# Kernel tuning notes

Hardware: AMD Instinct MI355X
Metric: run time of the kernel (lower is better)

Reference implementation:

```python
import jax, jax.numpy as jnp
import numpy as np

B, T, S, F_IN, F_OUT, K, L = 8, 8, 500, 32, 64, 3, 3


def setup_inputs() -> dict:
    key = jax.random.key(0)
    ks = jax.random.split(key, 10)
    x = jax.random.normal(ks[0], (B, T, S, F_IN), dtype=jnp.float32)
    Adj_t = jax.random.uniform(ks[1], (T, T), dtype=jnp.float32)
    Adj_s = jax.random.uniform(ks[2], (S, S), dtype=jnp.float32)
    # small mixing coefficients so Adj^k stays numerically tame
    s = jax.random.uniform(ks[3], (4,), dtype=jnp.float32) * 0.005
    H = jax.random.normal(ks[4], (L, K, F_OUT, F_OUT), dtype=jnp.float32) / jnp.sqrt(F_OUT)
    W1 = jax.random.normal(ks[5], (F_OUT, F_IN), dtype=jnp.float32) / jnp.sqrt(F_IN)
    b1 = jax.random.normal(ks[6], (F_OUT,), dtype=jnp.float32) * 0.01
    W2 = jax.random.normal(ks[7], (F_OUT, F_OUT), dtype=jnp.float32) / jnp.sqrt(F_OUT)
    b2 = jax.random.normal(ks[8], (F_OUT,), dtype=jnp.float32) * 0.01
    merge = jax.random.normal(ks[9], (T,), dtype=jnp.float32)
    return {"x": x, "Adj_t": Adj_t, "Adj_s": Adj_s, "s": s, "H": H,
            "W1": W1, "b1": b1, "W2": W2, "b2": b2, "merge": merge}


def reference(x, Adj_t, Adj_s, s, H, W1, b1, W2, b2, merge):
    Bx, Tx, Sx, Fin = x.shape
    N = Tx * Sx
    n_layers, Kk = H.shape[0], H.shape[1]
    I_t = jnp.eye(Tx, dtype=x.dtype)
    I_s = jnp.eye(Sx, dtype=x.dtype)
    I_st = jnp.eye(N, dtype=x.dtype)
    # mixed Kronecker product-graph adjacency, (T*S) x (T*S)
    Adj = (s[0] * I_st
           + s[1] * jnp.kron(I_t, Adj_s)
           + s[2] * jnp.kron(Adj_t, I_s)
           + s[3] * jnp.kron(Adj_t, Adj_s))
    # cache Adj^k for k = 0..K-1 (same math as per-layer matrix_power)
    powers = [I_st]
    for _ in range(1, Kk):
        powers.append(powers[-1] @ Adj)
    xf = x.reshape(Bx, N, Fin) @ W1.T + b1  # [B, N, F_out]
    for l in range(n_layers):
        acc = jnp.zeros_like(xf)
        for k in range(Kk):
            acc = acc + jnp.einsum('nm,bmf->bnf', powers[k], xf) @ H[l, k]
        xf = jnp.tanh(acc)
    xf = xf @ W2.T + b2  # [B, N, F_out]
    xo = xf.reshape(Bx, Tx, Sx, -1)  # [B, T, S, F_out]
    # transpose(3,1) -> [B,F,S,T]; matmul(merge) contracts T; transpose(2,1) -> [B,S,F]
    return jnp.einsum('btsf,t->bsf', xo, merge)
```

## Files before the change

kernel.cpp:

```cpp
#include <hip/hip_runtime.h>

#define BB 8
#define TT 8
#define SS 500
#define SP 512
#define FIN 32
#define FF 64
#define NBT 64
#define KT 1536
#define LROW_S 136
#define HROW 200
#define AROW 1544
#define WROW 196
#define OROW 520

typedef short bf16x8 __attribute__((ext_vector_type(8)));
typedef float floatx4 __attribute__((ext_vector_type(4)));

__device__ __forceinline__ unsigned f2bf(float x) {
    unsigned u = __builtin_bit_cast(unsigned, x);
    return (u + 0x7FFFu + ((u >> 16) & 1u)) >> 16;
}
__device__ __forceinline__ float bf2f(unsigned short h) {
    unsigned u = ((unsigned)h) << 16;
    return __builtin_bit_cast(float, u);
}
__device__ __forceinline__ float ftanh(float x) {
    float ax = fabsf(x);
    float e = __expf(-2.f * ax);
    float r = (1.f - e) * __builtin_amdgcn_rcpf(1.f + e);
    return copysignf(r, x);
}

__device__ __forceinline__ void ctab(int m, float s0, float s1, float s2, float s3,
                                     float& c0, float& c1, float& c2) {
    c0 = 0.f; c1 = 0.f; c2 = 0.f;
    switch (m) {
        case 0: c0 = 1.f; c1 = s0; c2 = s0 * s0; break;
        case 1: c1 = s1; c2 = 2.f * s0 * s1; break;
        case 2: c2 = s1 * s1; break;
        case 3: c1 = s2; c2 = 2.f * s0 * s2; break;
        case 4: c1 = s3; c2 = 2.f * (s0 * s3 + s1 * s2); break;
        case 5: c2 = 2.f * s1 * s3; break;
        case 6: c2 = s2 * s2; break;
        case 7: c2 = 2.f * s2 * s3; break;
        case 8: c2 = s3 * s3; break;
    }
}

__global__ __launch_bounds__(256) void setup_k(const float* __restrict__ x,
                                               const float* __restrict__ W1,
                                               const float* __restrict__ b1,
                                               const float* __restrict__ As,
                                               const float* __restrict__ At,
                                               const float* __restrict__ sc,
                                               const float* __restrict__ H,
                                               unsigned short* __restrict__ Asb,
                                               unsigned short* __restrict__ AsbT,
                                               unsigned short* __restrict__ HcT,
                                               float* __restrict__ CtT,
                                               unsigned short* __restrict__ xfT,
                                               unsigned short* __restrict__ Abig0) {
    int tid = threadIdx.x;
    if (blockIdx.x < 512) {
        __shared__ float Xs[64][FIN + 1];
        __shared__ float Wl[FIN][FF];
        __shared__ float Ot[64][FF + 1];
        __shared__ float bl[FF];
        int bt = blockIdx.x >> 3, s0 = (blockIdx.x & 7) * 64;
        int b = bt >> 3, t = bt & 7;

        for (int i = tid; i < FIN * FF; i += 256) { int f = i >> 5, j = i & 31; Wl[j][f] = W1[i]; }
        if (tid < FF) bl[tid] = b1[tid];
        const float* xb = x + (size_t)bt * SS * FIN;
        #pragma unroll
        for (int i = 0; i < 8; ++i) {
            int lin = i * 256 + tid; int r = lin >> 5, j = lin & 31;
            int s = s0 + r;
            Xs[r][j] = (s < SS) ? xb[(size_t)s * FIN + j] : 0.f;
        }
        __syncthreads();
        int f = tid & 63, sq = tid >> 6;
        for (int i = 0; i < 16; ++i) {
            int r = sq * 16 + i;
            float acc = bl[f];
            #pragma unroll
            for (int j = 0; j < FIN; ++j) acc += Xs[r][j] * Wl[j][f];
            Ot[r][f] = (s0 + r < SS) ? acc : 0.f;
        }
        __syncthreads();
        #pragma unroll
        for (int it = 0; it < 2; ++it) {
            int idx = it * 256 + tid;
            int row = idx >> 3, c = idx & 7;
            int4 w;
            unsigned short tmp[8];
            #pragma unroll
            for (int q = 0; q < 8; ++q) tmp[q] = (unsigned short)f2bf(Ot[row][c * 8 + q]);
            w.x = tmp[0] | (tmp[1] << 16); w.y = tmp[2] | (tmp[3] << 16);
            w.z = tmp[4] | (tmp[5] << 16); w.w = tmp[6] | (tmp[7] << 16);
            *(int4*)(Abig0 + (size_t)(b * SP + s0 + row) * KT + t * 192 + c * 8) = w;
        }
        {
            int ff = tid >> 2, scol = (tid & 3) * 16;
            unsigned short tmp[16];
            #pragma unroll
            for (int i = 0; i < 16; ++i) tmp[i] = (unsigned short)f2bf(Ot[scol + i][ff]);
            unsigned short* dp = xfT + ((size_t)bt * FF + ff) * SP + s0 + scol;
            #pragma unroll
            for (int q = 0; q < 2; ++q) {
                int4 w;
                w.x = tmp[q*8+0] | (tmp[q*8+1] << 16); w.y = tmp[q*8+2] | (tmp[q*8+3] << 16);
                w.z = tmp[q*8+4] | (tmp[q*8+5] << 16); w.w = tmp[q*8+6] | (tmp[q*8+7] << 16);
                *(int4*)(dp + q * 8) = w;
            }
        }
        return;
    }
    int idx = (blockIdx.x - 512) * 256 + tid;
    if (idx < 262144) {
        int s = idx >> 9, k = idx & 511;
        Asb[idx] = (s < SS && k < SS) ? (unsigned short)f2bf(As[(size_t)s * SS + k]) : 0;
    } else if (idx < 524288) {
        int r = idx - 262144;
        int j = r >> 9, k = r & 511;
        AsbT[r] = (j < SS && k < SS) ? (unsigned short)f2bf(As[(size_t)k * SS + j]) : 0;
    } else {
        int r = idx - 524288;
        if (r < 110592) {
            int l = r / 36864;
            int r2 = r - l * 36864;
            int row = r2 / 192;
            int col = r2 - row * 192;
            int p = row >> 6, f = row & 63;
            int bp = col >> 6, j = col & 63;
            float s0 = sc[0], s1 = sc[1], s2 = sc[2], s3 = sc[3];
            float c0, c1, c2;
            ctab(p * 3 + bp, s0, s1, s2, s3, c0, c1, c2);
            float val = c0 * H[((size_t)(l * 3 + 0) * 64 + j) * 64 + f]
                      + c1 * H[((size_t)(l * 3 + 1) * 64 + j) * 64 + f]
                      + c2 * H[((size_t)(l * 3 + 2) * 64 + j) * 64 + f];
            HcT[r] = (unsigned short)f2bf(val);
        } else if (r < 110784) {
            int i2 = r - 110592;
            int pt = i2 >> 3, t = i2 & 7;
            int p = pt >> 3, tp = pt & 7;
            float val;
            if (p == 0) val = (t == tp) ? 1.f : 0.f;
            else if (p == 1) val = At[t * 8 + tp];
            else {
                val = 0.f;
                #pragma unroll
                for (int kk = 0; kk < 8; ++kk) val += At[t * 8 + kk] * At[kk * 8 + tp];
            }
            CtT[i2] = val;
        }
    }
}

__global__ __launch_bounds__(256) void prep2_k(const unsigned short* __restrict__ Asb,
                                               const unsigned short* __restrict__ AsbT,
                                               unsigned short* __restrict__ Asqb) {
    int tid = threadIdx.x;
    int wave = tid >> 6, lane = tid & 63;
    int l16 = lane & 15, quad = lane >> 4;
    int st = blockIdx.x, ct = blockIdx.y;

    const unsigned short* ap = Asb + (size_t)(st * 16 + l16) * SP + quad * 8;
    const unsigned short* bp = AsbT + (size_t)(ct * 64 + wave * 16 + l16) * SP + quad * 8;
    floatx4 acc = {};
    #pragma unroll 4
    for (int k0 = 0; k0 < SP; k0 += 32)
        acc = __builtin_amdgcn_mfma_f32_16x16x32_bf16(*(const bf16x8*)(ap + k0),
                                                      *(const bf16x8*)(bp + k0), acc, 0, 0, 0);
    int j = ct * 64 + wave * 16 + l16;
    int i0 = st * 16 + quad * 4;
    #pragma unroll
    for (int r = 0; r < 4; ++r)
        Asqb[(size_t)(i0 + r) * SP + j] = (unsigned short)f2bf(acc[r]);
}

__global__ __launch_bounds__(256) void smm_k(const unsigned short* __restrict__ Asb,
                                             const unsigned short* __restrict__ Asqb,
                                             const unsigned short* __restrict__ xfT,
                                             unsigned short* __restrict__ Abig) {
    __shared__ unsigned short A1[64 * LROW_S];
    __shared__ unsigned short A2[64 * LROW_S];
    __shared__ unsigned short Bt[64 * LROW_S];

    int tid = threadIdx.x;
    int wave = tid >> 6, lane = tid & 63;
    int l16 = lane & 15, quad = lane >> 4;
    int m0 = blockIdx.x * 64, bt = blockIdx.y;
    int b = bt >> 3, t = bt & 7;

    const unsigned short* a1g = Asb + (size_t)m0 * SP;
    const unsigned short* a2g = Asqb + (size_t)m0 * SP;
    const unsigned short* bg  = xfT + (size_t)bt * FF * SP;

    floatx4 acc1[4] = {}, acc2[4] = {};

    for (int k0 = 0; k0 < SP; k0 += 128) {
        __syncthreads();
        #pragma unroll
        for (int it = 0; it < 4; ++it) {
            int idx = it * 256 + tid;
            int row = idx >> 4, c = idx & 15;
            int4 v1 = *(const int4*)(a1g + (size_t)row * SP + k0 + c * 8);
            int4 v2 = *(const int4*)(a2g + (size_t)row * SP + k0 + c * 8);
            int4 vb = *(const int4*)(bg  + (size_t)row * SP + k0 + c * 8);
            *(int4*)&A1[row * LROW_S + c * 8] = v1;
            *(int4*)&A2[row * LROW_S + c * 8] = v2;
            *(int4*)&Bt[row * LROW_S + c * 8] = vb;
        }
        __syncthreads();
        #pragma unroll
        for (int ks = 0; ks < 4; ++ks) {
            bf16x8 af1 = *(const bf16x8*)&A1[(wave * 16 + l16) * LROW_S + ks * 32 + quad * 8];
            bf16x8 af2 = *(const bf16x8*)&A2[(wave * 16 + l16) * LROW_S + ks * 32 + quad * 8];
            #pragma unroll
            for (int nt = 0; nt < 4; ++nt) {
                bf16x8 bf = *(const bf16x8*)&Bt[(nt * 16 + l16) * LROW_S + ks * 32 + quad * 8];
                acc1[nt] = __builtin_amdgcn_mfma_f32_16x16x32_bf16(af1, bf, acc1[nt], 0, 0, 0);
                acc2[nt] = __builtin_amdgcn_mfma_f32_16x16x32_bf16(af2, bf, acc2[nt], 0, 0, 0);
            }
        }
    }

    __syncthreads();
    #pragma unroll
    for (int nt = 0; nt < 4; ++nt)
        #pragma unroll
        for (int r = 0; r < 4; ++r) {
            A1[(wave * 16 + quad * 4 + r) * LROW_S + nt * 16 + l16] = (unsigned short)f2bf(acc1[nt][r]);
            A2[(wave * 16 + quad * 4 + r) * LROW_S + nt * 16 + l16] = (unsigned short)f2bf(acc2[nt][r]);
        }
    __syncthreads();
    int row = wave * 16 + (lane >> 2);
    int c2 = (lane & 3) * 2;
    #pragma unroll
    for (int q = 0; q < 2; ++q) {
        int c = c2 + q;
        int4 v1 = *(const int4*)&A1[row * LROW_S + c * 8];
        int4 v2 = *(const int4*)&A2[row * LROW_S + c * 8];
        size_t base = (size_t)(b * SP + m0 + row) * KT + t * 192;
        *(int4*)(Abig + base + 64 + c * 8)  = v1;
        *(int4*)(Abig + base + 128 + c * 8) = v2;
    }
}

__global__ __launch_bounds__(256) void hmix_k(const unsigned short* __restrict__ Abig,
                                              const unsigned short* __restrict__ HcT_l,
                                              const float* __restrict__ CtT,
                                              unsigned short* __restrict__ xfT_out,
                                              unsigned short* __restrict__ Abig_out,
                                              int wflag) {
    __shared__ int4 smem4[7888];
    __shared__ float CtS[192];
    unsigned short* As_ = (unsigned short*)smem4;
    unsigned short* Bs  = As_ + 16 * AROW;
    float* Wl = (float*)smem4;
    unsigned short* Ob = (unsigned short*)((char*)smem4 + 100352);

    int tid = threadIdx.x;
    int wave = tid >> 6, lane = tid & 63;
    int l16 = lane & 15, quad = lane >> 4;
    int wm = wave & 1, wn = wave >> 1;
    int s0 = blockIdx.x * 16, b = blockIdx.y;

    if (tid < 192) CtS[tid] = CtT[tid];

    {
        int ar = tid >> 4, ac = tid & 15;
        const unsigned short* agp = Abig + (size_t)(b * SP + s0 + ar) * KT;
        #pragma unroll
        for (int it = 0; it < 12; ++it) {
            int c = ac + it * 16;
            *(int4*)&As_[ar * AROW + c * 8] = *(const int4*)(agp + c * 8);
        }
    }
    {
        int br = tid >> 3, bc = tid & 7;
        #pragma unroll
        for (int it = 0; it < 6; ++it) {
            int row = it * 32 + br;
            const unsigned short* hp = HcT_l + (size_t)row * 192;
            #pragma unroll
            for (int j = 0; j < 3; ++j) {
                int c = bc + j * 8;
                *(int4*)&Bs[row * HROW + c * 8] = *(const int4*)(hp + c * 8);
            }
        }
    }
    __syncthreads();

    floatx4 acc[4][6] = {};
    #pragma unroll
    for (int ks = 0; ks < 6; ++ks) {
        bf16x8 af[4], bf[6];
        #pragma unroll
        for (int mt = 0; mt < 4; ++mt)
            af[mt] = *(const bf16x8*)&As_[l16 * AROW + (wm * 4 + mt) * 192 + ks * 32 + quad * 8];
        #pragma unroll
        for (int nt = 0; nt < 6; ++nt)
            bf[nt] = *(const bf16x8*)&Bs[((wn * 6 + nt) * 16 + l16) * HROW + ks * 32 + quad * 8];
        #pragma unroll
        for (int mt = 0; mt < 4; ++mt)
            #pragma unroll
            for (int nt = 0; nt < 6; ++nt)
                acc[mt][nt] = __builtin_amdgcn_mfma_f32_16x16x32_bf16(af[mt], bf[nt], acc[mt][nt], 0, 0, 0);
    }

    __syncthreads();
    #pragma unroll
    for (int mt = 0; mt < 4; ++mt)
        #pragma unroll
        for (int nt = 0; nt < 6; ++nt)
            #pragma unroll
            for (int r = 0; r < 4; ++r)
                Wl[((wm * 4 + mt) * 16 + quad * 4 + r) * WROW + (wn * 6 + nt) * 16 + l16] = acc[mt][nt][r];
    __syncthreads();

    {
        int f = tid & 63, sg = tid >> 6;
        float o[8][4] = {};
        #pragma unroll
        for (int pt = 0; pt < 24; ++pt) {
            int tp = pt & 7, p = pt >> 3;
            float wv[4];
            #pragma unroll
            for (int i = 0; i < 4; ++i)
                wv[i] = Wl[(tp * 16 + sg * 4 + i) * WROW + p * 64 + f];
            #pragma unroll
            for (int t = 0; t < 8; ++t) {
                float cv = CtS[pt * 8 + t];
                #pragma unroll
                for (int i = 0; i < 4; ++i) o[t][i] += cv * wv[i];
            }
        }
        #pragma unroll
        for (int t = 0; t < 8; ++t)
            #pragma unroll
            for (int i = 0; i < 4; ++i)
                Ob[(sg * 4 + i) * OROW + t * 64 + f] = (unsigned short)f2bf(ftanh(o[t][i]));
    }
    __syncthreads();

    #pragma unroll
    for (int it = 0; it < 4; ++it) {
        int u = it * 256 + tid;
        int sl = u >> 6, t = (u >> 3) & 7, c = u & 7;
        int4 v = *(const int4*)&Ob[sl * OROW + t * 64 + c * 8];
        *(int4*)(Abig_out + (size_t)(b * SP + s0 + sl) * KT + t * 192 + c * 8) = v;
    }
    if (wflag) {
        #pragma unroll
        for (int it = 0; it < 2; ++it) {
            int u = it * 256 + tid;
            int t = u >> 6, f = u & 63;
            unsigned short tmp[16];
            #pragma unroll
            for (int sl = 0; sl < 16; ++sl) tmp[sl] = Ob[sl * OROW + t * 64 + f];
            unsigned short* dp = xfT_out + ((size_t)(b * 8 + t) * FF + f) * SP + s0;
            #pragma unroll
            for (int q = 0; q < 2; ++q) {
                int4 w;
                w.x = tmp[q*8+0] | (tmp[q*8+1] << 16); w.y = tmp[q*8+2] | (tmp[q*8+3] << 16);
                w.z = tmp[q*8+4] | (tmp[q*8+5] << 16); w.w = tmp[q*8+6] | (tmp[q*8+7] << 16);
                *(int4*)(dp + q * 8) = w;
            }
        }
    }
}

__global__ __launch_bounds__(256) void zredlin2_k(const unsigned short* __restrict__ Abig,
                                                  const float* __restrict__ W2,
                                                  const float* __restrict__ b2,
                                                  const float* __restrict__ merge,
                                                  float* __restrict__ out) {
    __shared__ float Wl[FF][FF + 1];
    __shared__ float zt[16][FF + 1];
    __shared__ float ml[TT];
    int tid = threadIdx.x;
    int b = blockIdx.y, s0 = blockIdx.x * 16;

    for (int i = tid; i < FF * FF; i += 256) { int f = i >> 6, j = i & 63; Wl[j][f] = W2[i]; }
    if (tid < TT) ml[tid] = merge[tid];
    __syncthreads();

    float m[TT];
    #pragma unroll
    for (int t = 0; t < TT; ++t) m[t] = ml[t];
    float msum = 0.f;
    #pragma unroll
    for (int t = 0; t < TT; ++t) msum += m[t];

    #pragma unroll
    for (int p = 0; p < 4; ++p) {
        int lin = p * 256 + tid;
        int sl = lin >> 6, f = lin & 63;
        int s = s0 + sl;
        float acc = 0.f;
        if (s < SS) {
            #pragma unroll
            for (int t = 0; t < TT; ++t)
                acc += m[t] * bf2f(Abig[(size_t)(b * SP + s) * KT + t * 192 + f]);
        }
        zt[sl][f] = acc;
    }
    __syncthreads();

    int f = tid & 63, sq = tid >> 6;
    #pragma unroll
    for (int i = 0; i < 4; ++i) {
        int sl = sq * 4 + i;
        int s = s0 + sl;
        if (s < SS) {
            float acc = b2[f] * msum;
            #pragma unroll
            for (int j = 0; j < FF; ++j) acc += zt[sl][j] * Wl[j][f];
            out[((size_t)b * SS + s) * FF + f] = acc;
        }
    }
}

extern "C" void kernel_launch(void* const* d_in, const int* in_sizes, int n_in,
                              void* d_out, int out_size, void* d_ws, size_t ws_size,
                              hipStream_t stream) {
    const float* x     = (const float*)d_in[0];
    const float* At    = (const float*)d_in[1];
    const float* As    = (const float*)d_in[2];
    const float* sc    = (const float*)d_in[3];
    const float* H     = (const float*)d_in[4];
    const float* W1    = (const float*)d_in[5];
    const float* b1    = (const float*)d_in[6];
    const float* W2    = (const float*)d_in[7];
    const float* b2    = (const float*)d_in[8];
    const float* merge = (const float*)d_in[9];
    float* out = (float*)d_out;

    char* ws = (char*)d_ws;
    unsigned short* Asb   = (unsigned short*)(ws + 0);
    unsigned short* AsbT  = (unsigned short*)(ws + 524288);
    unsigned short* Asqb  = (unsigned short*)(ws + 1048576);
    unsigned short* HcT   = (unsigned short*)(ws + 1572864);
    float*          CtT   = (float*)(ws + 1794048);
    unsigned short* xfT0  = (unsigned short*)(ws + 6291456);
    unsigned short* xfT1  = (unsigned short*)(ws + 10485760);
    unsigned short* Abig0 = (unsigned short*)(ws + 14680064);
    unsigned short* Abig1 = (unsigned short*)(ws + 27262976);

    setup_k<<<2993, 256, 0, stream>>>(x, W1, b1, As, At, sc, H,
                                      Asb, AsbT, HcT, CtT, xfT0, Abig0);
    prep2_k<<<dim3(32, 8), 256, 0, stream>>>(Asb, AsbT, Asqb);

    unsigned short* xfT_cur = xfT0;  unsigned short* xfT_nxt = xfT1;
    unsigned short* Abig_cur = Abig0; unsigned short* Abig_nxt = Abig1;
    for (int l = 0; l < 3; ++l) {
        smm_k<<<dim3(8, NBT), 256, 0, stream>>>(Asb, Asqb, xfT_cur, Abig_cur);
        hmix_k<<<dim3(32, 8), 256, 0, stream>>>(Abig_cur,
                                                HcT + (size_t)l * 36864, CtT,
                                                xfT_nxt, Abig_nxt, (l < 2) ? 1 : 0);
        unsigned short* tt = xfT_cur;  xfT_cur = xfT_nxt;  xfT_nxt = tt;
        unsigned short* tb = Abig_cur; Abig_cur = Abig_nxt; Abig_nxt = tb;
    }
    zredlin2_k<<<dim3(32, 8), 256, 0, stream>>>(Abig_cur, W2, b2, merge, out);
}
```

Baseline: 165.6 us.

## Fuse final merge/W2 projection into last hmix layer and halve tile

Cuts hmix tile from 16 to 8 spatial rows, doubling the grid to 512 blocks. The A tile now goes straight from global memory into registers instead of through a large LDS staging buffer, which frees shared memory. On the last layer the merge-weighted reduction over time and the W2 linear run inside hmix, so one launch and the bf16 Abig write/read disappear. This may help occupancy and latency, at the cost of redundant H-tile loads per block and W2 loads in every final-layer block.

```diff
diff --git a/kernel.cpp b/kernel.cpp
--- a/kernel.cpp
+++ b/kernel.cpp
@@ -10,7 +10,6 @@
 #define KT 1536
 #define LROW_S 136
 #define HROW 200
-#define AROW 1544
 #define WROW 196
 #define OROW 520
 
@@ -252,33 +251,44 @@
 __global__ __launch_bounds__(256) void hmix_k(const unsigned short* __restrict__ Abig,
                                               const unsigned short* __restrict__ HcT_l,
                                               const float* __restrict__ CtT,
+                                              const float* __restrict__ W2,
+                                              const float* __restrict__ b2,
+                                              const float* __restrict__ merge,
                                               unsigned short* __restrict__ xfT_out,
                                               unsigned short* __restrict__ Abig_out,
+                                              float* __restrict__ out,
                                               int wflag) {
-    __shared__ int4 smem4[7888];
+    __shared__ char smem[76800];
     __shared__ float CtS[192];
-    unsigned short* As_ = (unsigned short*)smem4;
-    unsigned short* Bs  = As_ + 16 * AROW;
-    float* Wl = (float*)smem4;
-    unsigned short* Ob = (unsigned short*)((char*)smem4 + 100352);
+    __shared__ float mlS[8];
+    unsigned short* Bs  = (unsigned short*)smem;
+    float* Wl           = (float*)smem;
+    unsigned short* Ob  = (unsigned short*)(smem + 50176);
+    float* W2l          = (float*)(smem + 50176);
+    float* zt           = (float*)(smem + 66816);
 
     int tid = threadIdx.x;
     int wave = tid >> 6, lane = tid & 63;
     int l16 = lane & 15, quad = lane >> 4;
     int wm = wave & 1, wn = wave >> 1;
-    int s0 = blockIdx.x * 16, b = blockIdx.y;
+    int s0 = blockIdx.x * 8, b = blockIdx.y;
 
     if (tid < 192) CtS[tid] = CtT[tid];
-
+    if (tid < 8) mlS[tid] = merge[tid];
+
+    bf16x8 afr[2][6];
     {
-        int ar = tid >> 4, ac = tid & 15;
-        const unsigned short* agp = Abig + (size_t)(b * SP + s0 + ar) * KT;
-        #pragma unroll
-        for (int it = 0; it < 12; ++it) {
-            int c = ac + it * 16;
-            *(int4*)&As_[ar * AROW + c * 8] = *(const int4*)(agp + c * 8);
-        }
-    }
+        const unsigned short* abase =
+            Abig + (size_t)(b * SP + s0 + (l16 & 7)) * KT + quad * 8;
+        #pragma unroll
+        for (int mt = 0; mt < 2; ++mt) {
+            int tp = (wm * 2 + mt) * 2 + (l16 >> 3);
+            #pragma unroll
+            for (int ks = 0; ks < 6; ++ks)
+                afr[mt][ks] = *(const bf16x8*)(abase + tp * 192 + ks * 32);
+        }
+    }
+
     {
         int br = tid >> 3, bc = tid & 7;
         #pragma unroll
@@ -294,132 +304,113 @@
     }
     __syncthreads();
 
-    floatx4 acc[4][6] = {};
+    floatx4 acc[2][6] = {};
     #pragma unroll
     for (int ks = 0; ks < 6; ++ks) {
-        bf16x8 af[4], bf[6];
-        #pragma unroll
-        for (int mt = 0; mt < 4; ++mt)
-            af[mt] = *(const bf16x8*)&As_[l16 * AROW + (wm * 4 + mt) * 192 + ks * 32 + quad * 8];
+        bf16x8 bfr[6];
         #pragma unroll
         for (int nt = 0; nt < 6; ++nt)
-            bf[nt] = *(const bf16x8*)&Bs[((wn * 6 + nt) * 16 + l16) * HROW + ks * 32 + quad * 8];
-        #pragma unroll
-        for (int mt = 0; mt < 4; ++mt)
+            bfr[nt] = *(const bf16x8*)&Bs[((wn * 6 + nt) * 16 + l16) * HROW + ks * 32 + quad * 8];
+        #pragma unroll
+        for (int mt = 0; mt < 2; ++mt)
             #pragma unroll
             for (int nt = 0; nt < 6; ++nt)
-                acc[mt][nt] = __builtin_amdgcn_mfma_f32_16x16x32_bf16(af[mt], bf[nt], acc[mt][nt], 0, 0, 0);
+                acc[mt][nt] = __builtin_amdgcn_mfma_f32_16x16x32_bf16(afr[mt][ks], bfr[nt], acc[mt][nt], 0, 0, 0);
     }
 
     __syncthreads();
+
     #pragma unroll
-    for (int mt = 0; mt < 4; ++mt)
-        #pragma unroll
-        for (int nt = 0; nt < 6; ++nt)
-            #pragma unroll
-            for (int r = 0; r < 4; ++r)
-                Wl[((wm * 4 + mt) * 16 + quad * 4 + r) * WROW + (wn * 6 + nt) * 16 + l16] = acc[mt][nt][r];
+    for (int mt = 0; mt < 2; ++mt)
+        #pragma unroll
+        for (int nt = 0; nt < 6; ++nt) {
+            int col = (wn * 6 + nt) * 16 + l16;
+            #pragma unroll
+            for (int r = 0; r < 4; ++r) {
+                int fr = quad * 4 + r;
+                int tp = (wm * 2 + mt) * 2 + (fr >> 3);
+                int srow = fr & 7;
+                Wl[(tp * 8 + srow) * WROW + col] = acc[mt][nt][r];
+            }
+        }
+    if (!wflag) {
+        for (int i = tid; i < 4096; i += 256) { int f = i >> 6, j = i & 63; W2l[j * 65 + f] = W2[i]; }
+    }
     __syncthreads();
 
+    int f = tid & 63, sg = tid >> 6;
+    float th[8][2];
     {
-        int f = tid & 63, sg = tid >> 6;
-        float o[8][4] = {};
+        float o[8][2] = {};
         #pragma unroll
         for (int pt = 0; pt < 24; ++pt) {
             int tp = pt & 7, p = pt >> 3;
-            float wv[4];
-            #pragma unroll
-            for (int i = 0; i < 4; ++i)
-                wv[i] = Wl[(tp * 16 + sg * 4 + i) * WROW + p * 64 + f];
+            float w0 = Wl[(tp * 8 + sg * 2 + 0) * WROW + p * 64 + f];
+            float w1 = Wl[(tp * 8 + sg * 2 + 1) * WROW + p * 64 + f];
             #pragma unroll
             for (int t = 0; t < 8; ++t) {
                 float cv = CtS[pt * 8 + t];
-                #pragma unroll
-                for (int i = 0; i < 4; ++i) o[t][i] += cv * wv[i];
-            }
-        }
-        #pragma unroll
-        for (int t = 0; t < 8; ++t)
-            #pragma unroll
-            for (int i = 0; i < 4; ++i)
-                Ob[(sg * 4 + i) * OROW + t * 64 + f] = (unsigned short)f2bf(ftanh(o[t][i]));
-    }
-    __syncthreads();
-
-    #pragma unroll
-    for (int it = 0; it < 4; ++it) {
-        int u = it * 256 + tid;
-        int sl = u >> 6, t = (u >> 3) & 7, c = u & 7;
-        int4 v = *(const int4*)&Ob[sl * OROW + t * 64 + c * 8];
-        *(int4*)(Abig_out + (size_t)(b * SP + s0 + sl) * KT + t * 192 + c * 8) = v;
-    }
+                o[t][0] += cv * w0;
+                o[t][1] += cv * w1;
+            }
+        }
+        #pragma unroll
+        for (int t = 0; t < 8; ++t) {
+            th[t][0] = ftanh(o[t][0]);
+            th[t][1] = ftanh(o[t][1]);
+        }
+    }
+
     if (wflag) {
+        #pragma unroll
+        for (int t = 0; t < 8; ++t) {
+            Ob[(sg * 2 + 0) * OROW + t * 64 + f] = (unsigned short)f2bf(th[t][0]);
+            Ob[(sg * 2 + 1) * OROW + t * 64 + f] = (unsigned short)f2bf(th[t][1]);
+        }
+        __syncthreads();
+        #pragma unroll
+        for (int it = 0; it < 2; ++it) {
+            int idx = it * 256 + tid;
+            int row = idx >> 6, c = idx & 63;
+            int t = c >> 3, c8 = c & 7;
+            int4 v = *(const int4*)&Ob[row * OROW + c * 8];
+            *(int4*)(Abig_out + (size_t)(b * SP + s0 + row) * KT + t * 192 + c8 * 8) = v;
+        }
         #pragma unroll
         for (int it = 0; it < 2; ++it) {
             int u = it * 256 + tid;
-            int t = u >> 6, f = u & 63;
-            unsigned short tmp[16];
-            #pragma unroll
-            for (int sl = 0; sl < 16; ++sl) tmp[sl] = Ob[sl * OROW + t * 64 + f];
-            unsigned short* dp = xfT_out + ((size_t)(b * 8 + t) * FF + f) * SP + s0;
-            #pragma unroll
-            for (int q = 0; q < 2; ++q) {
-                int4 w;
-                w.x = tmp[q*8+0] | (tmp[q*8+1] << 16); w.y = tmp[q*8+2] | (tmp[q*8+3] << 16);
-                w.z = tmp[q*8+4] | (tmp[q*8+5] << 16); w.w = tmp[q*8+6] | (tmp[q*8+7] << 16);
-                *(int4*)(dp + q * 8) = w;
-            }
-        }
-    }
-}
-
-__global__ __launch_bounds__(256) void zredlin2_k(const unsigned short* __restrict__ Abig,
-                                                  const float* __restrict__ W2,
-                                                  const float* __restrict__ b2,
-                                                  const float* __restrict__ merge,
-                                                  float* __restrict__ out) {
-    __shared__ float Wl[FF][FF + 1];
-    __shared__ float zt[16][FF + 1];
-    __shared__ float ml[TT];
-    int tid = threadIdx.x;
-    int b = blockIdx.y, s0 = blockIdx.x * 16;
-
-    for (int i = tid; i < FF * FF; i += 256) { int f = i >> 6, j = i & 63; Wl[j][f] = W2[i]; }
-    if (tid < TT) ml[tid] = merge[tid];
-    __syncthreads();
-
-    float m[TT];
-    #pragma unroll
-    for (int t = 0; t < TT; ++t) m[t] = ml[t];
-    float msum = 0.f;
-    #pragma unroll
-    for (int t = 0; t < TT; ++t) msum += m[t];
-
-    #pragma unroll
-    for (int p = 0; p < 4; ++p) {
-        int lin = p * 256 + tid;
-        int sl = lin >> 6, f = lin & 63;
-        int s = s0 + sl;
-        float acc = 0.f;
-        if (s < SS) {
-            #pragma unroll
-            for (int t = 0; t < TT; ++t)
-                acc += m[t] * bf2f(Abig[(size_t)(b * SP + s) * KT + t * 192 + f]);
-        }
-        zt[sl][f] = acc;
-    }
-    __syncthreads();
-
-    int f = tid & 63, sq = tid >> 6;
-    #pragma unroll
-    for (int i = 0; i < 4; ++i) {
-        int sl = sq * 4 + i;
-        int s = s0 + sl;
-        if (s < SS) {
-            float acc = b2[f] * msum;
-            #pragma unroll
-            for (int j = 0; j < FF; ++j) acc += zt[sl][j] * Wl[j][f];
-            out[((size_t)b * SS + s) * FF + f] = acc;
+            int t = u >> 6, ff = u & 63;
+            unsigned short tmp[8];
+            #pragma unroll
+            for (int sl = 0; sl < 8; ++sl) tmp[sl] = Ob[sl * OROW + t * 64 + ff];
+            int4 w;
+            w.x = tmp[0] | (tmp[1] << 16); w.y = tmp[2] | (tmp[3] << 16);
+            w.z = tmp[4] | (tmp[5] << 16); w.w = tmp[6] | (tmp[7] << 16);
+            *(int4*)(xfT_out + ((size_t)(b * 8 + t) * FF + ff) * SP + s0) = w;
+        }
+    } else {
+        float z0 = 0.f, z1 = 0.f;
+        #pragma unroll
+        for (int t = 0; t < 8; ++t) {
+            z0 += mlS[t] * th[t][0];
+            z1 += mlS[t] * th[t][1];
+        }
+        zt[(sg * 2 + 0) * 65 + f] = z0;
+        zt[(sg * 2 + 1) * 65 + f] = z1;
+        __syncthreads();
+        float msum = 0.f;
+        #pragma unroll
+        for (int t = 0; t < 8; ++t) msum += mlS[t];
+        float bv = b2[f] * msum;
+        #pragma unroll
+        for (int r = 0; r < 2; ++r) {
+            int s = s0 + sg * 2 + r;
+            if (s < SS) {
+                float accv = bv;
+                #pragma unroll
+                for (int j = 0; j < FF; ++j) accv += zt[(sg * 2 + r) * 65 + j] * W2l[j * 65 + f];
+                out[((size_t)b * SS + s) * FF + f] = accv;
+            }
         }
     }
 }
@@ -458,11 +449,12 @@
     unsigned short* Abig_cur = Abig0; unsigned short* Abig_nxt = Abig1;
     for (int l = 0; l < 3; ++l) {
         smm_k<<<dim3(8, NBT), 256, 0, stream>>>(Asb, Asqb, xfT_cur, Abig_cur);
-        hmix_k<<<dim3(32, 8), 256, 0, stream>>>(Abig_cur,
+        hmix_k<<<dim3(64, 8), 256, 0, stream>>>(Abig_cur,
                                                 HcT + (size_t)l * 36864, CtT,
-                                                xfT_nxt, Abig_nxt, (l < 2) ? 1 : 0);
+                                                W2, b2, merge,
+                                                xfT_nxt, Abig_nxt, out,
+                                                (l < 2) ? 1 : 0);
         unsigned short* tt = xfT_cur;  xfT_cur = xfT_nxt;  xfT_nxt = tt;
         unsigned short* tb = Abig_cur; Abig_cur = Abig_nxt; Abig_nxt = tb;
     }
-    zredlin2_k<<<dim3(32, 8), 256, 0, stream>>>(Abig_cur, W2, b2, merge, out);
-}
+}
```

New measurement: 159.3 us. 3.8% less time.
